# Kernel tuning notes

Hardware: AMD Instinct MI355X
Metric: run time of the kernel (lower is better)

Reference implementation:

```python
import jax, jax.numpy as jnp
import numpy as np

N, E, F, B, S, T, D = 50000, 150000, 100000, 64, 32, 32, 3
RADIUS = 1.0
SCALE = 500.0


def setup_inputs() -> dict:
    key = jax.random.key(0)
    ks = jax.random.split(key, 8)
    x = jax.random.normal(ks[0], (N, D), dtype=jnp.float32)
    node_weights = jax.random.uniform(ks[1], (N,), dtype=jnp.float32)
    edge_index = jax.random.randint(ks[2], (2, E), 0, N)
    edge_weights = jax.random.uniform(ks[3], (E,), dtype=jnp.float32)
    face = jax.random.randint(ks[4], (3, F), 0, N)
    face_weights = jax.random.uniform(ks[5], (F,), dtype=jnp.float32)
    batch = jnp.sort(jax.random.randint(ks[6], (N,), 0, B))
    v = jax.random.normal(ks[7], (D, T), dtype=jnp.float32)
    v = v / jnp.linalg.norm(v, axis=0, keepdims=True)  # unit directions
    lin = jnp.linspace(-RADIUS, RADIUS, S, dtype=jnp.float32)
    return {"x": x, "node_weights": node_weights, "edge_index": edge_index,
            "edge_weights": edge_weights, "face": face, "face_weights": face_weights,
            "batch": batch, "v": v, "lin": lin}


def compute_ecc(h, index, lin, num_segments):
    # h: [M, T] simplex heights; lin: [S] thresholds
    # sigmoid bump at each threshold, then scatter-add per graph -> [B, S, T]
    ecc = jax.nn.sigmoid(SCALE * (lin[None, :, None] - h[:, None, :]))  # [M, S, T]
    return jax.ops.segment_sum(ecc, index, num_segments=num_segments)


def reference(x, node_weights, edge_index, edge_weights, face, face_weights, batch, v, lin):
    nh = (x * node_weights[:, None]) @ v                      # [N, T] node heights
    eh = jnp.max(nh[edge_index], axis=0) * edge_weights[:, None]  # [E, T]
    fh = jnp.max(nh[face], axis=0) * face_weights[:, None]        # [F, T]
    idx_e = batch[edge_index[0]]
    idx_f = batch[face[0]]
    ect = (compute_ecc(nh, batch, lin, B)
           - compute_ecc(eh, idx_e, lin, B)
           + compute_ecc(fh, idx_f, lin, B))                  # [B, S, T]
    return ect  # normalized=False -> squeeze() is a no-op here
```

## Files before the change

kernel.cpp:

```cpp
#include <hip/hip_runtime.h>
#include <hip/hip_bf16.h>

#define N_NODES 50000
#define N_EDGES 150000
#define N_FACES 100000
#define NB 64
#define NS 32
#define NT 32
#define SCALE_C 500.0f
#define DLIN (2.0f / 31.0f)
#define INV_DLIN (31.0f / 2.0f)
#define WIN 0.02f
#define DSZ (NB * NS * NT)
#define CH 128
#define NODE_CAP 1152
#define EDGE_CAP 3072
#define FACE_CAP 2048

__device__ __forceinline__ float sigf(float z) {
    float e = __expf(-z);
    return __builtin_amdgcn_rcpf(1.0f + e);
}

__global__ __launch_bounds__(256) void prep_kernel(
    const float* __restrict__ x, const float* __restrict__ nw,
    const float* __restrict__ v, const int* __restrict__ ei,
    const float* __restrict__ ew, const int* __restrict__ fi,
    const float* __restrict__ fw, const int* __restrict__ batch,
    float* __restrict__ nh, int* __restrict__ ns,
    int* __restrict__ ea, int* __restrict__ eb, float* __restrict__ ews,
    int* __restrict__ fa, int* __restrict__ fb, int* __restrict__ fc,
    float* __restrict__ fws, int* __restrict__ cur,
    int nhB, int nbN, int nbE)
{
    if (blockIdx.x < nhB) {
        int idx = blockIdx.x * 256 + threadIdx.x;
        if (idx < N_NODES * NT) {
            int n = idx >> 5, t = idx & 31;
            float w = nw[n];
            nh[idx] = w * (x[3 * n] * v[t] + x[3 * n + 1] * v[NT + t] + x[3 * n + 2] * v[2 * NT + t]);
        }
        return;
    }
    __shared__ int cnt[NB], base_[NB];
    int b = blockIdx.x - nhB;
    int type, bb, M;
    if (b < nbN)            { type = 0; bb = b;             M = N_NODES; }
    else if (b < nbN + nbE) { type = 1; bb = b - nbN;       M = N_EDGES; }
    else                    { type = 2; bb = b - nbN - nbE; M = N_FACES; }
    int c0 = bb * 1024;
    if (threadIdx.x < NB) cnt[threadIdx.x] = 0;
    __syncthreads();
    int gv[4], iv[4], n = 0;
    #pragma unroll
    for (int k = 0; k < 4; k++) {
        int i = c0 + k * 256 + threadIdx.x;
        if (i < M) {
            int first = (type == 0) ? i : (type == 1 ? ei[i] : fi[i]);
            gv[n] = batch[first];
            iv[n] = i;
            atomicAdd(&cnt[gv[n]], 1);
            n++;
        }
    }
    __syncthreads();
    int* curT = cur + type * NB;
    if (threadIdx.x < NB) {
        base_[threadIdx.x] = atomicAdd(&curT[threadIdx.x], cnt[threadIdx.x]);
        cnt[threadIdx.x] = 0;
    }
    __syncthreads();
    int CAP = (type == 0) ? NODE_CAP : (type == 1 ? EDGE_CAP : FACE_CAP);
    for (int k = 0; k < n; k++) {
        int g = gv[k], i = iv[k];
        int pos = g * CAP + base_[g] + atomicAdd(&cnt[g], 1);
        if (type == 0) {
            ns[pos] = i;
        } else if (type == 1) {
            ea[pos] = ei[i]; eb[pos] = ei[N_EDGES + i]; ews[pos] = ew[i];
        } else {
            fa[pos] = fi[i]; fb[pos] = fi[N_FACES + i];
            fc[pos] = fi[2 * N_FACES + i]; fws[pos] = fw[i];
        }
    }
}

__global__ __launch_bounds__(256) void accum_kernel(
    const float* __restrict__ nh, const int* __restrict__ ns,
    const int* __restrict__ ea, const int* __restrict__ eb,
    const float* __restrict__ ews, const int* __restrict__ fa,
    const int* __restrict__ fb, const int* __restrict__ fc,
    const float* __restrict__ fws, const int* __restrict__ cur,
    float* __restrict__ delta)
{
    const int NBN = NB * NODE_CAP / CH;
    const int NBE = NB * EDGE_CAP / CH;
    int t = threadIdx.x & 31, slot = threadIdx.x >> 5;
    int bid = blockIdx.x;
    int type, g, i0, end;
    float sign;
    if (bid < NBN) {
        type = 0; int r = bid * CH; g = r / NODE_CAP; i0 = r;
        end = g * NODE_CAP + cur[g]; sign = 1.0f;
    } else if (bid < NBN + NBE) {
        type = 1; int r = (bid - NBN) * CH; g = r / EDGE_CAP; i0 = r;
        end = g * EDGE_CAP + cur[NB + g]; sign = -1.0f;
    } else {
        type = 2; int r = (bid - NBN - NBE) * CH; g = r / FACE_CAP; i0 = r;
        end = g * FACE_CAP + cur[2 * NB + g]; sign = 1.0f;
    }
    if (i0 >= end) return;
    int i1 = min(i0 + CH, end);

    __shared__ float tile[NS * NT];
    for (int k = threadIdx.x; k < NS * NT; k += 256) tile[k] = 0.0f;
    __syncthreads();

    for (int base = i0 + slot; base < i1; base += 32) {
        float h[4];
        #pragma unroll
        for (int k = 0; k < 4; k++) {
            int i = base + k * 8;
            if (i < i1) {
                if (type == 0)
                    h[k] = nh[ns[i] * NT + t];
                else if (type == 1)
                    h[k] = fmaxf(nh[ea[i] * NT + t], nh[eb[i] * NT + t]) * ews[i];
                else
                    h[k] = fmaxf(fmaxf(nh[fa[i] * NT + t], nh[fb[i] * NT + t]),
                                 nh[fc[i] * NT + t]) * fws[i];
            }
        }
        #pragma unroll
        for (int k = 0; k < 4; k++) {
            int i = base + k * 8;
            if (i < i1) {
                float hh = h[k];
                int slo_u = (int)ceilf((hh - WIN + 1.0f) * INV_DLIN);
                int shi_u = (int)floorf((hh + WIN + 1.0f) * INV_DLIN);
                int slo = slo_u < 0 ? 0 : slo_u;
                int shi = shi_u > (NS - 1) ? (NS - 1) : shi_u;
                float prev = 0.0f;
                for (int s = slo; s <= shi; s++) {
                    float vs = sigf(SCALE_C * (-1.0f + s * DLIN - hh));
                    atomicAdd(&tile[s * NT + t], vs - prev);
                    prev = vs;
                }
                int sstep = shi_u + 1;
                if (sstep <= NS - 1) {
                    int sc = sstep < 0 ? 0 : sstep;
                    atomicAdd(&tile[sc * NT + t], 1.0f - prev);
                }
            }
        }
    }

    __syncthreads();
    for (int k = threadIdx.x; k < NS * NT; k += 256) {
        float vv = tile[k];
        if (vv != 0.0f) atomicAdd(&delta[g * (NS * NT) + k], sign * vv);
    }
}

__global__ void finalize_kernel(const float* __restrict__ delta, float* __restrict__ out) {
    int idx = blockIdx.x * blockDim.x + threadIdx.x;
    if (idx >= NB * NT) return;
    int g = idx >> 5, t = idx & 31;
    const float* dg = delta + (g * NS) * NT + t;
    float* og = out + (g * NS) * NT + t;
    float run = 0.0f;
    for (int s = 0; s < NS; s++) {
        run += dg[s * NT];
        og[s * NT] = run;
    }
}

extern "C" void kernel_launch(void* const* d_in, const int* in_sizes, int n_in,
                              void* d_out, int out_size, void* d_ws, size_t ws_size,
                              hipStream_t stream) {
    const float* x     = (const float*)d_in[0];
    const float* nw    = (const float*)d_in[1];
    const int*   ei    = (const int*)d_in[2];
    const float* ew    = (const float*)d_in[3];
    const int*   fi    = (const int*)d_in[4];
    const float* fw    = (const float*)d_in[5];
    const int*   batch = (const int*)d_in[6];
    const float* v     = (const float*)d_in[7];
    const float* lin   = (const float*)d_in[8];
    (void)lin; (void)in_sizes; (void)n_in; (void)ws_size;
    float* out = (float*)d_out;

    char* ws = (char*)d_ws;
    float* delta = (float*)ws;
    int*   cur   = (int*)(ws + DSZ * 4);
    float* nh    = (float*)(ws + DSZ * 4 + 1024);
    int*   ns    = (int*)((char*)nh + (size_t)N_NODES * NT * 4);
    int*   ea    = ns + NB * NODE_CAP;
    int*   eb    = ea + NB * EDGE_CAP;
    float* ews   = (float*)(eb + NB * EDGE_CAP);
    int*   fa    = (int*)(ews + NB * EDGE_CAP);
    int*   fb    = fa + NB * FACE_CAP;
    int*   fc    = fb + NB * FACE_CAP;
    float* fws   = (float*)(fc + NB * FACE_CAP);

    hipMemsetAsync(delta, 0, DSZ * 4 + 1024, stream);

    int nhB = (N_NODES * NT + 255) / 256;
    int nbN = (N_NODES + 1023) / 1024;
    int nbE = (N_EDGES + 1023) / 1024;
    int nbF = (N_FACES + 1023) / 1024;
    prep_kernel<<<nhB + nbN + nbE + nbF, 256, 0, stream>>>(
        x, nw, v, ei, ew, fi, fw, batch,
        nh, ns, ea, eb, ews, fa, fb, fc, fws, cur, nhB, nbN, nbE);

    int nblk = NB * (NODE_CAP + EDGE_CAP + FACE_CAP) / CH;
    accum_kernel<<<nblk, 256, 0, stream>>>(
        nh, ns, ea, eb, ews, fa, fb, fc, fws, cur, delta);

    finalize_kernel<<<(NB * NT + 255) / 256, 256, 0, stream>>>(delta, out);
}
```

Measured before the change: 195.8 us.

## Vectorize height gathers with float4 and pad simplex lists with sentinel node

Each thread now gathers 8 consecutive direction heights per simplex via float4 loads instead of one scalar per thread, and the shared histogram is transposed to [t][s]. Bucket lists are pre-filled by a new fill kernel with a sentinel node whose height lies outside the threshold range, removing per-element bounds checks. Blocks now process 256 simplices each and the node capacity is reduced. This adds an extra kernel launch and may introduce LDS bank conflicts on the transposed tile atomics.

```diff
diff --git a/kernel.cpp b/kernel.cpp
--- a/kernel.cpp
+++ b/kernel.cpp
@@ -12,14 +12,33 @@
 #define INV_DLIN (31.0f / 2.0f)
 #define WIN 0.02f
 #define DSZ (NB * NS * NT)
-#define CH 128
-#define NODE_CAP 1152
+#define NODE_CAP 1024
 #define EDGE_CAP 3072
 #define FACE_CAP 2048
+#define SENT_H 2.0f
 
 __device__ __forceinline__ float sigf(float z) {
     float e = __expf(-z);
     return __builtin_amdgcn_rcpf(1.0f + e);
+}
+__device__ __forceinline__ float4 fmax4(float4 a, float4 b) {
+    return make_float4(fmaxf(a.x,b.x), fmaxf(a.y,b.y), fmaxf(a.z,b.z), fmaxf(a.w,b.w));
+}
+__device__ __forceinline__ float4 fscale4(float4 a, float w) {
+    return make_float4(a.x*w, a.y*w, a.z*w, a.w*w);
+}
+
+__global__ __launch_bounds__(256) void fill_kernel(
+    float* __restrict__ nh, int* __restrict__ ns,
+    int* __restrict__ ea, int* __restrict__ eb, float* __restrict__ ews,
+    int* __restrict__ fa, int* __restrict__ fb, int* __restrict__ fc,
+    float* __restrict__ fws)
+{
+    int i = blockIdx.x * 256 + threadIdx.x;
+    if (i < NT) nh[N_NODES * NT + i] = SENT_H;
+    if (i < NB * NODE_CAP) ns[i] = N_NODES;
+    if (i < NB * EDGE_CAP) { ea[i] = N_NODES; eb[i] = N_NODES; ews[i] = 1.0f; }
+    if (i < NB * FACE_CAP) { fa[i] = N_NODES; fb[i] = N_NODES; fc[i] = N_NODES; fws[i] = 1.0f; }
 }
 
 __global__ __launch_bounds__(256) void prep_kernel(
@@ -93,72 +112,85 @@
     const float* __restrict__ fws, const int* __restrict__ cur,
     float* __restrict__ delta)
 {
-    const int NBN = NB * NODE_CAP / CH;
-    const int NBE = NB * EDGE_CAP / CH;
-    int t = threadIdx.x & 31, slot = threadIdx.x >> 5;
+    const int NBN = NB * NODE_CAP / 256;
+    const int NBE = NB * EDGE_CAP / 256;
     int bid = blockIdx.x;
-    int type, g, i0, end;
+    int type, g, base, end;
     float sign;
     if (bid < NBN) {
-        type = 0; int r = bid * CH; g = r / NODE_CAP; i0 = r;
+        type = 0; g = bid >> 2; base = g * NODE_CAP + (bid & 3) * 256;
         end = g * NODE_CAP + cur[g]; sign = 1.0f;
     } else if (bid < NBN + NBE) {
-        type = 1; int r = (bid - NBN) * CH; g = r / EDGE_CAP; i0 = r;
+        int b = bid - NBN; type = 1; g = b / 12;
+        base = g * EDGE_CAP + (b % 12) * 256;
         end = g * EDGE_CAP + cur[NB + g]; sign = -1.0f;
     } else {
-        type = 2; int r = (bid - NBN - NBE) * CH; g = r / FACE_CAP; i0 = r;
+        int b = bid - NBN - NBE; type = 2; g = b >> 3;
+        base = g * FACE_CAP + (b & 7) * 256;
         end = g * FACE_CAP + cur[2 * NB + g]; sign = 1.0f;
     }
-    if (i0 >= end) return;
-    int i1 = min(i0 + CH, end);
-
-    __shared__ float tile[NS * NT];
-    for (int k = threadIdx.x; k < NS * NT; k += 256) tile[k] = 0.0f;
-    __syncthreads();
-
-    for (int base = i0 + slot; base < i1; base += 32) {
-        float h[4];
+    if (base >= end) return;
+
+    __shared__ float tile[NT * NS];
+    for (int k = threadIdx.x; k < NT * NS; k += 256) tile[k] = 0.0f;
+    __syncthreads();
+
+    int sub = threadIdx.x & 3;
+    int sid = threadIdx.x >> 2;
+    int t0 = sub * 8;
+
+    #pragma unroll
+    for (int p = 0; p < 4; p++) {
+        int i = base + p * 64 + sid;
+        float4 r0, r1;
+        if (type == 0) {
+            const float4* row = (const float4*)(nh + ns[i] * NT + t0);
+            r0 = row[0]; r1 = row[1];
+        } else if (type == 1) {
+            const float4* ra = (const float4*)(nh + ea[i] * NT + t0);
+            const float4* rb = (const float4*)(nh + eb[i] * NT + t0);
+            float w = ews[i];
+            float4 a0 = ra[0], a1 = ra[1], b0 = rb[0], b1 = rb[1];
+            r0 = fscale4(fmax4(a0, b0), w);
+            r1 = fscale4(fmax4(a1, b1), w);
+        } else {
+            const float4* ra = (const float4*)(nh + fa[i] * NT + t0);
+            const float4* rb = (const float4*)(nh + fb[i] * NT + t0);
+            const float4* rc = (const float4*)(nh + fc[i] * NT + t0);
+            float w = fws[i];
+            float4 a0 = ra[0], a1 = ra[1], b0 = rb[0], b1 = rb[1], c0 = rc[0], c1 = rc[1];
+            r0 = fscale4(fmax4(fmax4(a0, b0), c0), w);
+            r1 = fscale4(fmax4(fmax4(a1, b1), c1), w);
+        }
+        float h[8] = {r0.x, r0.y, r0.z, r0.w, r1.x, r1.y, r1.z, r1.w};
         #pragma unroll
-        for (int k = 0; k < 4; k++) {
-            int i = base + k * 8;
-            if (i < i1) {
-                if (type == 0)
-                    h[k] = nh[ns[i] * NT + t];
-                else if (type == 1)
-                    h[k] = fmaxf(nh[ea[i] * NT + t], nh[eb[i] * NT + t]) * ews[i];
-                else
-                    h[k] = fmaxf(fmaxf(nh[fa[i] * NT + t], nh[fb[i] * NT + t]),
-                                 nh[fc[i] * NT + t]) * fws[i];
+        for (int j = 0; j < 8; j++) {
+            float hh = h[j];
+            int slo_u = (int)ceilf((hh - WIN + 1.0f) * INV_DLIN);
+            int shi_u = (int)floorf((hh + WIN + 1.0f) * INV_DLIN);
+            int slo = slo_u < 0 ? 0 : slo_u;
+            int shi = shi_u > (NS - 1) ? (NS - 1) : shi_u;
+            float prev = 0.0f;
+            for (int s = slo; s <= shi; s++) {
+                float vs = sigf(SCALE_C * (-1.0f + s * DLIN - hh));
+                atomicAdd(&tile[(t0 + j) * NS + s], vs - prev);
+                prev = vs;
             }
-        }
-        #pragma unroll
-        for (int k = 0; k < 4; k++) {
-            int i = base + k * 8;
-            if (i < i1) {
-                float hh = h[k];
-                int slo_u = (int)ceilf((hh - WIN + 1.0f) * INV_DLIN);
-                int shi_u = (int)floorf((hh + WIN + 1.0f) * INV_DLIN);
-                int slo = slo_u < 0 ? 0 : slo_u;
-                int shi = shi_u > (NS - 1) ? (NS - 1) : shi_u;
-                float prev = 0.0f;
-                for (int s = slo; s <= shi; s++) {
-                    float vs = sigf(SCALE_C * (-1.0f + s * DLIN - hh));
-                    atomicAdd(&tile[s * NT + t], vs - prev);
-                    prev = vs;
-                }
-                int sstep = shi_u + 1;
-                if (sstep <= NS - 1) {
-                    int sc = sstep < 0 ? 0 : sstep;
-                    atomicAdd(&tile[sc * NT + t], 1.0f - prev);
-                }
+            int sstep = shi_u + 1;
+            if (sstep <= NS - 1) {
+                int sc = sstep < 0 ? 0 : sstep;
+                atomicAdd(&tile[(t0 + j) * NS + sc], 1.0f - prev);
             }
         }
     }
 
     __syncthreads();
-    for (int k = threadIdx.x; k < NS * NT; k += 256) {
+    for (int k = threadIdx.x; k < NT * NS; k += 256) {
         float vv = tile[k];
-        if (vv != 0.0f) atomicAdd(&delta[g * (NS * NT) + k], sign * vv);
+        if (vv != 0.0f) {
+            int tt = k >> 5, ss = k & 31;
+            atomicAdd(&delta[g * (NS * NT) + ss * NT + tt], sign * vv);
+        }
     }
 }
 
@@ -194,7 +226,7 @@
     float* delta = (float*)ws;
     int*   cur   = (int*)(ws + DSZ * 4);
     float* nh    = (float*)(ws + DSZ * 4 + 1024);
-    int*   ns    = (int*)((char*)nh + (size_t)N_NODES * NT * 4);
+    int*   ns    = (int*)((char*)nh + (size_t)(N_NODES + 1) * NT * 4);
     int*   ea    = ns + NB * NODE_CAP;
     int*   eb    = ea + NB * EDGE_CAP;
     float* ews   = (float*)(eb + NB * EDGE_CAP);
@@ -205,6 +237,8 @@
 
     hipMemsetAsync(delta, 0, DSZ * 4 + 1024, stream);
 
+    fill_kernel<<<NB * EDGE_CAP / 256, 256, 0, stream>>>(nh, ns, ea, eb, ews, fa, fb, fc, fws);
+
     int nhB = (N_NODES * NT + 255) / 256;
     int nbN = (N_NODES + 1023) / 1024;
     int nbE = (N_EDGES + 1023) / 1024;
@@ -213,7 +247,7 @@
         x, nw, v, ei, ew, fi, fw, batch,
         nh, ns, ea, eb, ews, fa, fb, fc, fws, cur, nhB, nbN, nbE);
 
-    int nblk = NB * (NODE_CAP + EDGE_CAP + FACE_CAP) / CH;
+    int nblk = NB * (NODE_CAP + EDGE_CAP + FACE_CAP) / 256;
     accum_kernel<<<nblk, 256, 0, stream>>>(
         nh, ns, ea, eb, ews, fa, fb, fc, fws, cur, delta);
 
```

Measured after the change: 195.1 us. Within noise of the previous version (-0.4%).
